# Optimization experiments

Hardware: AMD Instinct MI355X
Metric: run time of the kernel (lower is better)

## Reference

```python
import jax, jax.numpy as jnp
import numpy as np

B, N, DIM = 2, 2048, 1024
NUM_HEADS = 16
EFF = NUM_HEADS // 2          # 8 effective heads
HD = DIM // NUM_HEADS         # 64
LAMBDA_INIT = 0.8
EPS = 1e-5


def setup_inputs() -> dict:
    key = jax.random.key(0)
    ks = jax.random.split(key, 16)
    s = 0.02
    return {
        "x":  jax.random.normal(ks[0], (B, N, DIM), dtype=jnp.float32),
        "Wq": jax.random.normal(ks[1], (DIM, DIM), dtype=jnp.float32) * s,
        "bq": jnp.zeros((DIM,), dtype=jnp.float32),
        "Wk": jax.random.normal(ks[2], (DIM, DIM), dtype=jnp.float32) * s,
        "bk": jnp.zeros((DIM,), dtype=jnp.float32),
        "Wv": jax.random.normal(ks[3], (DIM, DIM), dtype=jnp.float32) * s,
        "bv": jnp.zeros((DIM,), dtype=jnp.float32),
        "Wo": jax.random.normal(ks[4], (DIM, DIM), dtype=jnp.float32) * s,
        "bo": jnp.zeros((DIM,), dtype=jnp.float32),
        "norm_w": jnp.ones((2 * HD,), dtype=jnp.float32),
        "lq1": jax.random.normal(ks[5], (HD,), dtype=jnp.float32) * 0.1,
        "lk1": jax.random.normal(ks[6], (HD,), dtype=jnp.float32) * 0.1,
        "lq2": jax.random.normal(ks[7], (HD,), dtype=jnp.float32) * 0.1,
        "lk2": jax.random.normal(ks[8], (HD,), dtype=jnp.float32) * 0.1,
    }


def reference(x, Wq, bq, Wk, bk, Wv, bv, Wo, bo, norm_w, lq1, lk1, lq2, lk2):
    scale = HD ** -0.5
    # projections (torch Linear: y = x @ W.T + b)
    q = (x @ Wq.T + bq).reshape(B, N, NUM_HEADS, HD).transpose(0, 2, 1, 3) * scale  # [B,2E,N,hd]
    k = (x @ Wk.T + bk).reshape(B, N, NUM_HEADS, HD).transpose(0, 2, 1, 3)          # [B,2E,N,hd]
    v = (x @ Wv.T + bv).reshape(B, N, EFF, 2 * HD).transpose(0, 2, 1, 3)            # [B,E,N,2hd]

    scores = jnp.einsum('bhqd,bhkd->bhqk', q, k)              # [B,2E,N,N]
    probs = jax.nn.softmax(scores, axis=-1)
    probs = probs.reshape(B, EFF, 2, N, N)                    # pair consecutive heads

    lam = jnp.exp(jnp.sum(lq1 * lk1)) - jnp.exp(jnp.sum(lq2 * lk2)) + LAMBDA_INIT
    diff = probs[:, :, 0] - lam * probs[:, :, 1]              # [B,E,N,N]

    out = jnp.einsum('behk,bekd->behd'.replace('e','h').replace('hh','h') if False else 'bhqk,bhkd->bhqd', diff, v)  # [B,E,N,2hd]
    # headwise RMSNorm over last dim (2*hd)
    out = out * jax.lax.rsqrt(jnp.mean(out * out, axis=-1, keepdims=True) + EPS) * norm_w
    out = out * (1.0 - LAMBDA_INIT)

    out = out.transpose(0, 2, 1, 3).reshape(B, N, DIM)
    return out @ Wo.T + bo
```

## Files before the change

kernel.cpp:

```cpp
#include <hip/hip_runtime.h>
#include <hip/hip_bf16.h>

#define B_   2
#define N_   2048
#define DIM_ 1024
#define HD_  64
#define DV_  128

typedef __bf16 bf16;
typedef __bf16 bf16x8 __attribute__((ext_vector_type(8)));
typedef __bf16 bf16x4 __attribute__((ext_vector_type(4)));
typedef float  floatx4 __attribute__((ext_vector_type(4)));
typedef float  floatx16 __attribute__((ext_vector_type(16)));
typedef unsigned int uint;
typedef uint uint2v __attribute__((ext_vector_type(2)));
typedef uint uint4v __attribute__((ext_vector_type(4)));

#if __has_builtin(__builtin_amdgcn_exp2f)
#define EXP2(x) __builtin_amdgcn_exp2f(x)
#else
#define EXP2(x) exp2f(x)
#endif

#define QSCALE 0.1803368801111244f

__device__ __forceinline__ void async16(const void* g, void* l) {
  __builtin_amdgcn_global_load_lds(
      (__attribute__((address_space(1))) void*)g,
      (__attribute__((address_space(3))) void*)l, 16, 0, 0);
}

__device__ __forceinline__ uint packbf(float a, float b) {
  unsigned short ul = __builtin_bit_cast(unsigned short, (bf16)a);
  unsigned short uh = __builtin_bit_cast(unsigned short, (bf16)b);
  return (uint)ul | ((uint)uh << 16);
}

__global__ void convert_kernel(const float* __restrict__ x,
                               const float* __restrict__ wq,
                               const float* __restrict__ wk,
                               const float* __restrict__ wv,
                               const float* __restrict__ wo,
                               bf16* __restrict__ dst) {
  const int NX = B_ * N_ * DIM_;
  const int NW = DIM_ * DIM_;
  int i = (blockIdx.x * 256 + threadIdx.x) * 4;
  const float* src;
  int off;
  if (i < NX) { src = x; off = i; }
  else {
    int j = i - NX;
    int w = j >> 20;
    off = j & (NW - 1);
    src = (w == 0) ? wq : (w == 1) ? wk : (w == 2) ? wv : wo;
  }
  float4 v = *(const float4*)(src + off);
  bf16x4 o = { (bf16)v.x, (bf16)v.y, (bf16)v.z, (bf16)v.w };
  *(bf16x4*)(dst + i) = o;
}

__global__ void lam_kernel(const float* __restrict__ lq1, const float* __restrict__ lk1,
                           const float* __restrict__ lq2, const float* __restrict__ lk2,
                           float* __restrict__ lam_out) {
  int l = threadIdx.x;
  float a = lq1[l] * lk1[l];
  float b = lq2[l] * lk2[l];
  for (int m = 1; m < 64; m <<= 1) {
    a += __shfl_xor(a, m, 64);
    b += __shfl_xor(b, m, 64);
  }
  if (l == 0) *lam_out = __expf(a) - __expf(b) + 0.8f;
}

__global__ __launch_bounds__(256) void proj_kernel(
    const bf16* __restrict__ xb, const bf16* __restrict__ wall,
    const float* __restrict__ bq, const float* __restrict__ bk,
    const float* __restrict__ bv,
    bf16* __restrict__ qo, bf16* __restrict__ ko, bf16* __restrict__ vt) {
  __shared__ __align__(16) bf16 SM[2 * 128 * 64];
  bf16* At = SM;
  bf16* Bt = SM + 128 * 64;
  const int tid = threadIdx.x, lane = tid & 63, w = tid >> 6;
  const int tm = blockIdx.x, tn = blockIdx.y, z = blockIdx.z;
  const int quad = lane >> 4, l15 = lane & 15;
  const int wm = (w >> 1) * 64, wn = (w & 1) * 64;
  const bf16* Ab = xb + (long)tm * 128 * DIM_;
  const bf16* Bb = wall + (long)z * (DIM_ * DIM_) + (long)tn * 128 * DIM_;
  floatx4 zero = {0.f, 0.f, 0.f, 0.f};
  floatx4 acc[4][4];
#pragma unroll
  for (int i = 0; i < 4; ++i)
#pragma unroll
    for (int j = 0; j < 4; ++j) acc[i][j] = zero;

  for (int kb = 0; kb < DIM_ / 64; ++kb) {
    for (int idx = tid; idx < 1024; idx += 256) {
      int row = idx >> 3, ch = idx & 7, g = ch ^ (row & 7);
      async16(Ab + row * DIM_ + kb * 64 + g * 8, (char*)At + (idx - lane) * 16);
      async16(Bb + row * DIM_ + kb * 64 + g * 8, (char*)Bt + (idx - lane) * 16);
    }
    __syncthreads();
#pragma unroll
    for (int ks = 0; ks < 2; ++ks) {
      bf16x8 af[4], bfm[4];
#pragma unroll
      for (int mt = 0; mt < 4; ++mt) {
        int r = wm + mt * 16 + l15;
        af[mt] = *(const bf16x8*)&At[r * 64 + ((ks * 4 + quad) ^ (r & 7)) * 8];
      }
#pragma unroll
      for (int nt = 0; nt < 4; ++nt) {
        int r = wn + nt * 16 + l15;
        bfm[nt] = *(const bf16x8*)&Bt[r * 64 + ((ks * 4 + quad) ^ (r & 7)) * 8];
      }
#pragma unroll
      for (int mt = 0; mt < 4; ++mt)
#pragma unroll
        for (int nt = 0; nt < 4; ++nt)
          acc[mt][nt] = __builtin_amdgcn_mfma_f32_16x16x32_bf16(
              af[mt], bfm[nt], acc[mt][nt], 0, 0, 0);
    }
    __syncthreads();
  }

  if (z != 2) {
#pragma unroll
    for (int mt = 0; mt < 4; ++mt)
#pragma unroll
      for (int nt = 0; nt < 4; ++nt)
#pragma unroll
        for (int r = 0; r < 4; ++r) {
          int grow = tm * 128 + wm + mt * 16 + quad * 4 + r;
          int gcol = tn * 128 + wn + nt * 16 + l15;
          float v = acc[mt][nt][r];
          if (z == 0) {
            qo[(long)grow * DIM_ + gcol] = (bf16)((v + bq[gcol]) * QSCALE);
          } else {
            ko[(long)grow * DIM_ + gcol] = (bf16)(v + bk[gcol]);
          }
        }
  } else {
    bf16* Vl = SM;
#pragma unroll
    for (int nt = 0; nt < 4; ++nt) {
      int d = wn + nt * 16 + l15;
      float bvv = bv[tn * 128 + d];
      int m = (d & 7) * 2;
#pragma unroll
      for (int mt = 0; mt < 4; ++mt) {
        bf16x4 v4 = { (bf16)(acc[mt][nt][0] + bvv), (bf16)(acc[mt][nt][1] + bvv),
                      (bf16)(acc[mt][nt][2] + bvv), (bf16)(acc[mt][nt][3] + bvv) };
        int c = (wm >> 2) + mt * 4 + quad;
        *(bf16x4*)&Vl[d * 128 + (c ^ m) * 4] = v4;
      }
    }
    __syncthreads();
    const int bb = tm >> 4, e = tn;
    const long rowbase = ((long)(bb * 8 + e) * 128) * (long)N_ + (tm & 15) * 128;
#pragma unroll
    for (int p = 0; p < 8; ++p) {
      int d = p * 16 + (tid >> 4), j = tid & 15;
      int cs = (2 * j) ^ ((d & 7) * 2);
      bf16x8 val = *(const bf16x8*)&Vl[d * 128 + cs * 4];
      *(bf16x8*)&vt[rowbase + (long)d * N_ + j * 8] = val;
    }
  }
}

__global__ __launch_bounds__(1024, 4) void attn_kernel(
    const bf16* __restrict__ qb, const bf16* __restrict__ kbuf,
    const bf16* __restrict__ vt, const float* __restrict__ lamp,
    const float* __restrict__ norm_w, bf16* __restrict__ ao) {
  __shared__ __align__(16) char smem[131072];
  __shared__ float Ls[512];

  const int tid = threadIdx.x, lane = tid & 63, w = tid >> 6;
  const int qt = blockIdx.x, e = blockIdx.y, b = blockIdx.z;
  const int hl = w & 1, qh = (w >> 1) & 3, cp = w >> 3;
  const int h = lane >> 5, l31 = lane & 31;
  const int qbase = qt * 128;

  bf16x8 qf[4];
  {
    const bf16* qrp = qb + (long)(b * N_ + qbase + qh * 32 + l31) * DIM_
                      + e * 128 + hl * 64 + h * 8;
#pragma unroll
    for (int c = 0; c < 4; ++c) qf[c] = *(const bf16x8*)(qrp + c * 16);
  }

  const bf16* kbase = kbuf + (long)b * N_ * DIM_ + e * 128;
  const bf16* vbase = vt + (long)(b * 8 + e) * DV_ * N_;

  floatx16 acc[4];
#pragma unroll
  for (int dt = 0; dt < 4; ++dt) acc[dt] = floatx16{};
  float lp = 0.f;

#define STAGE(ktv, bufv)                                                            \
  {                                                                                 \
    int kt_ = (ktv);                                                                \
    char* kdst = smem + (bufv) * 16384;                                             \
    char* vdst = smem + 32768 + (bufv) * 16384;                                     \
    {                                                                               \
      int idx = tid;                                                                \
      int khl = idx >> 9, row = (idx >> 3) & 63, ch = idx & 7;                      \
      int g = ch ^ (row & 7) ^ ((row >> 3) & 3);                                    \
      async16(kbase + ((long)(kt_ * 64 + row)) * DIM_ + khl * 64 + g * 8,           \
              kdst + (idx - lane) * 16);                                            \
    }                                                                               \
    {                                                                               \
      int idx = tid;                                                                \
      int row = idx >> 3, ch = idx & 7;                                             \
      int g = ch ^ (row & 7) ^ ((row >> 3) & 3);                                    \
      async16(vbase + (long)row * N_ + kt_ * 64 + g * 8,                            \
              vdst + (idx - lane) * 16);                                            \
    }                                                                               \
  }

  STAGE(0, 0);

  for (int kt = 0; kt < N_ / 64; ++kt) {
    const int buf = kt & 1;
    __syncthreads();
    if (kt + 1 < N_ / 64) STAGE(kt + 1, buf ^ 1);

    const bf16* Kh = (const bf16*)(smem + buf * 16384) + hl * 4096;
    const bf16* Vb = (const bf16*)(smem + 32768 + buf * 16384);

    bf16x8 kfrag[4], vfrag[4][2];
#pragma unroll
    for (int c = 0; c < 4; ++c) {
      int row = cp * 32 + l31;
      int sw = (c * 2 + h) ^ (row & 7) ^ ((row >> 3) & 3);
      kfrag[c] = *(const bf16x8*)&Kh[row * 64 + sw * 8];
    }
#pragma unroll
    for (int dt = 0; dt < 4; ++dt)
#pragma unroll
      for (int u = 0; u < 2; ++u) {
        int kc = cp * 2 + u;
        int row = dt * 32 + l31;
        int sw = (kc * 2 + h) ^ (row & 7) ^ ((row >> 3) & 3);
        vfrag[dt][u] = *(const bf16x8*)&Vb[row * 64 + sw * 8];
      }

    floatx16 sv{};
#pragma unroll
    for (int c = 0; c < 4; ++c)
      sv = __builtin_amdgcn_mfma_f32_32x32x16_bf16(kfrag[c], qf[c], sv, 0, 0, 0);
    float t[16];
    float s = 0.f;
#pragma unroll
    for (int i = 0; i < 16; ++i) { t[i] = EXP2(sv[i]); s += t[i]; }
    lp += s;
    uint d0 = packbf(t[0], t[1]),   d1 = packbf(t[2], t[3]);
    uint d2 = packbf(t[4], t[5]),   d3 = packbf(t[6], t[7]);
    uint d4 = packbf(t[8], t[9]),   d5 = packbf(t[10], t[11]);
    uint d6 = packbf(t[12], t[13]), d7 = packbf(t[14], t[15]);
    uint4v f0, f1;
#if __has_builtin(__builtin_amdgcn_permlane32_swap)
    uint2v r02 = __builtin_amdgcn_permlane32_swap(d0, d2, false, false);
    uint2v r13 = __builtin_amdgcn_permlane32_swap(d1, d3, false, false);
    f0 = uint4v{r02.x, r13.x, r02.y, r13.y};
    uint2v r46 = __builtin_amdgcn_permlane32_swap(d4, d6, false, false);
    uint2v r57 = __builtin_amdgcn_permlane32_swap(d5, d7, false, false);
    f1 = uint4v{r46.x, r57.x, r46.y, r57.y};
#else
    uint e0 = __shfl_xor((int)d0, 32, 64), e1 = __shfl_xor((int)d1, 32, 64);
    uint e2 = __shfl_xor((int)d2, 32, 64), e3 = __shfl_xor((int)d3, 32, 64);
    uint e4 = __shfl_xor((int)d4, 32, 64), e5 = __shfl_xor((int)d5, 32, 64);
    uint e6 = __shfl_xor((int)d6, 32, 64), e7 = __shfl_xor((int)d7, 32, 64);
    f0 = h ? uint4v{e2, e3, d2, d3} : uint4v{d0, d1, e0, e1};
    f1 = h ? uint4v{e6, e7, d6, d7} : uint4v{d4, d5, e4, e5};
#endif
    bf16x8 af0 = __builtin_bit_cast(bf16x8, f0);
    bf16x8 af1 = __builtin_bit_cast(bf16x8, f1);
#pragma unroll
    for (int dt = 0; dt < 4; ++dt) {
      acc[dt] = __builtin_amdgcn_mfma_f32_32x32x16_bf16(af0, vfrag[dt][0], acc[dt], 0, 0, 0);
      acc[dt] = __builtin_amdgcn_mfma_f32_32x32x16_bf16(af1, vfrag[dt][1], acc[dt], 0, 0, 0);
    }
  }

  lp += __shfl_xor(lp, 32, 64);
  if (h == 0) Ls[cp * 256 + hl * 128 + qh * 32 + l31] = lp;
  __syncthreads();
  float lptot = Ls[hl * 128 + qh * 32 + l31] + Ls[256 + hl * 128 + qh * 32 + l31];

  float* S = (float*)smem;
  float* T = (float*)(smem + 65536);

  if (hl == 1 && cp == 0) {
#pragma unroll
    for (int r = 0; r < 16; ++r) {
      int qloc = (r & 3) + 8 * (r >> 2) + 4 * h;
      float inv = 1.0f / __shfl(lptot, qloc, 64);
      float* row = &S[(qh * 32 + qloc) * 128 + l31];
#pragma unroll
      for (int dt = 0; dt < 4; ++dt) row[dt * 32] = acc[dt][r] * inv;
    }
  }
  if (hl == 0 && cp == 1) {
#pragma unroll
    for (int r = 0; r < 16; ++r) {
      int qloc = (r & 3) + 8 * (r >> 2) + 4 * h;
      float inv = 1.0f / __shfl(lptot, qloc, 64);
      float* row = &T[(qh * 32 + qloc) * 128 + l31];
#pragma unroll
      for (int dt = 0; dt < 4; ++dt) row[dt * 32] = acc[dt][r] * inv;
    }
  }
  __syncthreads();
  if (hl == 1 && cp == 1) {
#pragma unroll
    for (int r = 0; r < 16; ++r) {
      int qloc = (r & 3) + 8 * (r >> 2) + 4 * h;
      float inv = 1.0f / __shfl(lptot, qloc, 64);
      float* row = &S[(qh * 32 + qloc) * 128 + l31];
#pragma unroll
      for (int dt = 0; dt < 4; ++dt) row[dt * 32] += acc[dt][r] * inv;
    }
  }
  if (hl == 0 && cp == 0) {
#pragma unroll
    for (int r = 0; r < 16; ++r) {
      int qloc = (r & 3) + 8 * (r >> 2) + 4 * h;
      float inv = 1.0f / __shfl(lptot, qloc, 64);
      const float* row = &T[(qh * 32 + qloc) * 128 + l31];
#pragma unroll
      for (int dt = 0; dt < 4; ++dt) acc[dt][r] = acc[dt][r] * inv + row[dt * 32];
    }
  }
  __syncthreads();
  if (hl == 0 && cp == 0) {
    float lam = *lamp;
    float nw4[4];
#pragma unroll
    for (int dt = 0; dt < 4; ++dt) nw4[dt] = norm_w[dt * 32 + l31] * 0.2f;
#pragma unroll
    for (int r = 0; r < 16; ++r) {
      int qloc = (r & 3) + 8 * (r >> 2) + 4 * h;
      const float* row = &S[(qh * 32 + qloc) * 128 + l31];
      float v[4], ss = 0.f;
#pragma unroll
      for (int dt = 0; dt < 4; ++dt) {
        v[dt] = acc[dt][r] - lam * row[dt * 32];
        ss += v[dt] * v[dt];
      }
#pragma unroll
      for (int msk = 1; msk < 32; msk <<= 1) ss += __shfl_xor(ss, msk, 64);
      float rms = rsqrtf(ss * (1.0f / 128.0f) + 1e-5f);
      int n = qbase + qh * 32 + qloc;
      bf16* dst = ao + (long)(b * N_ + n) * DIM_ + e * DV_ + l31;
#pragma unroll
      for (int dt = 0; dt < 4; ++dt) dst[dt * 32] = (bf16)(v[dt] * rms * nw4[dt]);
    }
  }
}

__global__ __launch_bounds__(512) void out_gemm(
    const bf16* __restrict__ ab, const bf16* __restrict__ wo,
    const float* __restrict__ bo, float* __restrict__ out) {
  __shared__ __align__(16) bf16 At[128 * 64];
  __shared__ __align__(16) bf16 Bt[128 * 64];
  const int tid = threadIdx.x, lane = tid & 63, w = tid >> 6;
  const int tm = blockIdx.x, tn = blockIdx.y;
  const int quad = lane >> 4, l15 = lane & 15;
  const int wm = (w & 3) * 32, wn = (w >> 2) * 64;
  const bf16* Ab = ab + (long)tm * 128 * DIM_;
  const bf16* Bb = wo + (long)tn * 128 * DIM_;
  floatx4 zero = {0.f, 0.f, 0.f, 0.f};
  floatx4 acc[2][4];
#pragma unroll
  for (int i = 0; i < 2; ++i)
#pragma unroll
    for (int j = 0; j < 4; ++j) acc[i][j] = zero;

  for (int kb = 0; kb < DIM_ / 64; ++kb) {
    for (int idx = tid; idx < 1024; idx += 512) {
      int row = idx >> 3, ch = idx & 7, g = ch ^ (row & 7);
      async16(Ab + row * DIM_ + kb * 64 + g * 8, (char*)At + (idx - lane) * 16);
      async16(Bb + row * DIM_ + kb * 64 + g * 8, (char*)Bt + (idx - lane) * 16);
    }
    __syncthreads();
#pragma unroll
    for (int ks = 0; ks < 2; ++ks) {
      bf16x8 af[2], bfm[4];
#pragma unroll
      for (int mt = 0; mt < 2; ++mt) {
        int r = wm + mt * 16 + l15;
        af[mt] = *(const bf16x8*)&At[r * 64 + ((ks * 4 + quad) ^ (r & 7)) * 8];
      }
#pragma unroll
      for (int nt = 0; nt < 4; ++nt) {
        int r = wn + nt * 16 + l15;
        bfm[nt] = *(const bf16x8*)&Bt[r * 64 + ((ks * 4 + quad) ^ (r & 7)) * 8];
      }
#pragma unroll
      for (int mt = 0; mt < 2; ++mt)
#pragma unroll
        for (int nt = 0; nt < 4; ++nt)
          acc[mt][nt] = __builtin_amdgcn_mfma_f32_16x16x32_bf16(
              af[mt], bfm[nt], acc[mt][nt], 0, 0, 0);
    }
    __syncthreads();
  }
#pragma unroll
  for (int mt = 0; mt < 2; ++mt)
#pragma unroll
    for (int nt = 0; nt < 4; ++nt)
#pragma unroll
      for (int r = 0; r < 4; ++r) {
        int grow = tm * 128 + wm + mt * 16 + quad * 4 + r;
        int gcol = tn * 128 + wn + nt * 16 + l15;
        out[(long)grow * DIM_ + gcol] = acc[mt][nt][r] + bo[gcol];
      }
}

extern "C" void kernel_launch(void* const* d_in, const int* in_sizes, int n_in,
                              void* d_out, int out_size, void* d_ws, size_t ws_size,
                              hipStream_t stream) {
  const float* x    = (const float*)d_in[0];
  const float* Wq   = (const float*)d_in[1];
  const float* bq   = (const float*)d_in[2];
  const float* Wk   = (const float*)d_in[3];
  const float* bk   = (const float*)d_in[4];
  const float* Wv   = (const float*)d_in[5];
  const float* bv   = (const float*)d_in[6];
  const float* Wo   = (const float*)d_in[7];
  const float* bo   = (const float*)d_in[8];
  const float* nw   = (const float*)d_in[9];
  const float* lq1  = (const float*)d_in[10];
  const float* lk1  = (const float*)d_in[11];
  const float* lq2  = (const float*)d_in[12];
  const float* lk2  = (const float*)d_in[13];

  char* ws = (char*)d_ws;
  float* lam = (float*)ws;
  bf16* xb   = (bf16*)(ws + 256);
  bf16* wqb  = xb + 4194304;
  bf16* qb   = wqb + 4 * 1048576;
  bf16* kbuf = qb + 4194304;
  bf16* vtb  = kbuf + 4194304;
  bf16* ab   = vtb + 4194304;

  convert_kernel<<<8192, 256, 0, stream>>>(x, Wq, Wk, Wv, Wo, xb);
  lam_kernel<<<1, 64, 0, stream>>>(lq1, lk1, lq2, lk2, lam);
  proj_kernel<<<dim3(32, 8, 3), 256, 0, stream>>>(xb, wqb, bq, bk, bv, qb, kbuf, vtb);
  attn_kernel<<<dim3(16, 8, 2), 1024, 0, stream>>>(qb, kbuf, vtb, lam, nw, ab);
  out_gemm<<<dim3(32, 8), 512, 0, stream>>>(ab, wqb + 3 * 1048576, bo, (float*)d_out);
}
```

Measured before the change: 217.7 us.

## Halve attention block to 512 threads, each wave handling two query subtiles

The attention kernel drops from 16 to 8 waves per block, and each wave now processes two 32-row query subtiles against the same K/V fragments loaded from LDS. This amortizes the LDS fragment reads across twice the MFMA work and halves the number of waves contending for barriers. In exchange, each wave holds twice the accumulator and Q registers, which may limit occupancy or cause spills. The grid stays at 256 blocks, so there are fewer total waves to hide latency.

```diff
diff --git a/kernel.cpp b/kernel.cpp
--- a/kernel.cpp
+++ b/kernel.cpp
@@ -167,7 +167,7 @@
   }
 }
 
-__global__ __launch_bounds__(1024, 4) void attn_kernel(
+__global__ __launch_bounds__(512, 2) void attn_kernel(
     const bf16* __restrict__ qb, const bf16* __restrict__ kbuf,
     const bf16* __restrict__ vt, const float* __restrict__ lamp,
     const float* __restrict__ norm_w, bf16* __restrict__ ao) {
@@ -176,40 +176,43 @@
 
   const int tid = threadIdx.x, lane = tid & 63, w = tid >> 6;
   const int qt = blockIdx.x, e = blockIdx.y, b = blockIdx.z;
-  const int hl = w & 1, qh = (w >> 1) & 3, cp = w >> 3;
+  const int hl = w & 1, qh = (w >> 1) & 1, cp = w >> 2;
   const int h = lane >> 5, l31 = lane & 31;
   const int qbase = qt * 128;
 
-  bf16x8 qf[4];
-  {
-    const bf16* qrp = qb + (long)(b * N_ + qbase + qh * 32 + l31) * DIM_
+  bf16x8 qf[2][4];
+#pragma unroll
+  for (int qs = 0; qs < 2; ++qs) {
+    const bf16* qrp = qb + (long)(b * N_ + qbase + qh * 64 + qs * 32 + l31) * DIM_
                       + e * 128 + hl * 64 + h * 8;
 #pragma unroll
-    for (int c = 0; c < 4; ++c) qf[c] = *(const bf16x8*)(qrp + c * 16);
+    for (int c = 0; c < 4; ++c) qf[qs][c] = *(const bf16x8*)(qrp + c * 16);
   }
 
   const bf16* kbase = kbuf + (long)b * N_ * DIM_ + e * 128;
   const bf16* vbase = vt + (long)(b * 8 + e) * DV_ * N_;
 
-  floatx16 acc[4];
-#pragma unroll
-  for (int dt = 0; dt < 4; ++dt) acc[dt] = floatx16{};
-  float lp = 0.f;
+  floatx16 acc[2][4];
+#pragma unroll
+  for (int qs = 0; qs < 2; ++qs)
+#pragma unroll
+    for (int dt = 0; dt < 4; ++dt) acc[qs][dt] = floatx16{};
+  float lp[2] = {0.f, 0.f};
 
 #define STAGE(ktv, bufv)                                                            \
   {                                                                                 \
     int kt_ = (ktv);                                                                \
     char* kdst = smem + (bufv) * 16384;                                             \
     char* vdst = smem + 32768 + (bufv) * 16384;                                     \
-    {                                                                               \
-      int idx = tid;                                                                \
+    _Pragma("unroll") for (int t = 0; t < 2; ++t) {                                 \
+      int idx = tid + t * 512;                                                      \
       int khl = idx >> 9, row = (idx >> 3) & 63, ch = idx & 7;                      \
       int g = ch ^ (row & 7) ^ ((row >> 3) & 3);                                    \
       async16(kbase + ((long)(kt_ * 64 + row)) * DIM_ + khl * 64 + g * 8,           \
               kdst + (idx - lane) * 16);                                            \
     }                                                                               \
-    {                                                                               \
-      int idx = tid;                                                                \
+    _Pragma("unroll") for (int t = 0; t < 2; ++t) {                                 \
+      int idx = tid + t * 512;                                                      \
       int row = idx >> 3, ch = idx & 7;                                             \
       int g = ch ^ (row & 7) ^ ((row >> 3) & 3);                                    \
       async16(vbase + (long)row * N_ + kt_ * 64 + g * 8,                            \
@@ -244,92 +247,111 @@
         vfrag[dt][u] = *(const bf16x8*)&Vb[row * 64 + sw * 8];
       }
 
-    floatx16 sv{};
-#pragma unroll
-    for (int c = 0; c < 4; ++c)
-      sv = __builtin_amdgcn_mfma_f32_32x32x16_bf16(kfrag[c], qf[c], sv, 0, 0, 0);
-    float t[16];
-    float s = 0.f;
-#pragma unroll
-    for (int i = 0; i < 16; ++i) { t[i] = EXP2(sv[i]); s += t[i]; }
-    lp += s;
-    uint d0 = packbf(t[0], t[1]),   d1 = packbf(t[2], t[3]);
-    uint d2 = packbf(t[4], t[5]),   d3 = packbf(t[6], t[7]);
-    uint d4 = packbf(t[8], t[9]),   d5 = packbf(t[10], t[11]);
-    uint d6 = packbf(t[12], t[13]), d7 = packbf(t[14], t[15]);
-    uint4v f0, f1;
+#pragma unroll
+    for (int qs = 0; qs < 2; ++qs) {
+      floatx16 sv{};
+#pragma unroll
+      for (int c = 0; c < 4; ++c)
+        sv = __builtin_amdgcn_mfma_f32_32x32x16_bf16(kfrag[c], qf[qs][c], sv, 0, 0, 0);
+      float t[16];
+      float s = 0.f;
+#pragma unroll
+      for (int i = 0; i < 16; ++i) { t[i] = EXP2(sv[i]); s += t[i]; }
+      lp[qs] += s;
+      uint d0 = packbf(t[0], t[1]),   d1 = packbf(t[2], t[3]);
+      uint d2 = packbf(t[4], t[5]),   d3 = packbf(t[6], t[7]);
+      uint d4 = packbf(t[8], t[9]),   d5 = packbf(t[10], t[11]);
+      uint d6 = packbf(t[12], t[13]), d7 = packbf(t[14], t[15]);
+      uint4v f0, f1;
 #if __has_builtin(__builtin_amdgcn_permlane32_swap)
-    uint2v r02 = __builtin_amdgcn_permlane32_swap(d0, d2, false, false);
-    uint2v r13 = __builtin_amdgcn_permlane32_swap(d1, d3, false, false);
-    f0 = uint4v{r02.x, r13.x, r02.y, r13.y};
-    uint2v r46 = __builtin_amdgcn_permlane32_swap(d4, d6, false, false);
-    uint2v r57 = __builtin_amdgcn_permlane32_swap(d5, d7, false, false);
-    f1 = uint4v{r46.x, r57.x, r46.y, r57.y};
+      uint2v r02 = __builtin_amdgcn_permlane32_swap(d0, d2, false, false);
+      uint2v r13 = __builtin_amdgcn_permlane32_swap(d1, d3, false, false);
+      f0 = uint4v{r02.x, r13.x, r02.y, r13.y};
+      uint2v r46 = __builtin_amdgcn_permlane32_swap(d4, d6, false, false);
+      uint2v r57 = __builtin_amdgcn_permlane32_swap(d5, d7, false, false);
+      f1 = uint4v{r46.x, r57.x, r46.y, r57.y};
 #else
-    uint e0 = __shfl_xor((int)d0, 32, 64), e1 = __shfl_xor((int)d1, 32, 64);
-    uint e2 = __shfl_xor((int)d2, 32, 64), e3 = __shfl_xor((int)d3, 32, 64);
-    uint e4 = __shfl_xor((int)d4, 32, 64), e5 = __shfl_xor((int)d5, 32, 64);
-    uint e6 = __shfl_xor((int)d6, 32, 64), e7 = __shfl_xor((int)d7, 32, 64);
-    f0 = h ? uint4v{e2, e3, d2, d3} : uint4v{d0, d1, e0, e1};
-    f1 = h ? uint4v{e6, e7, d6, d7} : uint4v{d4, d5, e4, e5};
+      uint e0 = __shfl_xor((int)d0, 32, 64), e1 = __shfl_xor((int)d1, 32, 64);
+      uint e2 = __shfl_xor((int)d2, 32, 64), e3 = __shfl_xor((int)d3, 32, 64);
+      uint e4 = __shfl_xor((int)d4, 32, 64), e5 = __shfl_xor((int)d5, 32, 64);
+      uint e6 = __shfl_xor((int)d6, 32, 64), e7 = __shfl_xor((int)d7, 32, 64);
+      f0 = h ? uint4v{e2, e3, d2, d3} : uint4v{d0, d1, e0, e1};
+      f1 = h ? uint4v{e6, e7, d6, d7} : uint4v{d4, d5, e4, e5};
 #endif
-    bf16x8 af0 = __builtin_bit_cast(bf16x8, f0);
-    bf16x8 af1 = __builtin_bit_cast(bf16x8, f1);
-#pragma unroll
-    for (int dt = 0; dt < 4; ++dt) {
-      acc[dt] = __builtin_amdgcn_mfma_f32_32x32x16_bf16(af0, vfrag[dt][0], acc[dt], 0, 0, 0);
-      acc[dt] = __builtin_amdgcn_mfma_f32_32x32x16_bf16(af1, vfrag[dt][1], acc[dt], 0, 0, 0);
-    }
-  }
-
-  lp += __shfl_xor(lp, 32, 64);
-  if (h == 0) Ls[cp * 256 + hl * 128 + qh * 32 + l31] = lp;
+      bf16x8 af0 = __builtin_bit_cast(bf16x8, f0);
+      bf16x8 af1 = __builtin_bit_cast(bf16x8, f1);
+#pragma unroll
+      for (int dt = 0; dt < 4; ++dt) {
+        acc[qs][dt] = __builtin_amdgcn_mfma_f32_32x32x16_bf16(af0, vfrag[dt][0], acc[qs][dt], 0, 0, 0);
+        acc[qs][dt] = __builtin_amdgcn_mfma_f32_32x32x16_bf16(af1, vfrag[dt][1], acc[qs][dt], 0, 0, 0);
+      }
+    }
+  }
+
+  lp[0] += __shfl_xor(lp[0], 32, 64);
+  lp[1] += __shfl_xor(lp[1], 32, 64);
+  if (h == 0) {
+    Ls[cp * 256 + hl * 128 + qh * 64 + 0 * 32 + l31] = lp[0];
+    Ls[cp * 256 + hl * 128 + qh * 64 + 1 * 32 + l31] = lp[1];
+  }
   __syncthreads();
-  float lptot = Ls[hl * 128 + qh * 32 + l31] + Ls[256 + hl * 128 + qh * 32 + l31];
+  float lptot[2];
+#pragma unroll
+  for (int qs = 0; qs < 2; ++qs)
+    lptot[qs] = Ls[hl * 128 + qh * 64 + qs * 32 + l31]
+              + Ls[256 + hl * 128 + qh * 64 + qs * 32 + l31];
 
   float* S = (float*)smem;
   float* T = (float*)(smem + 65536);
 
   if (hl == 1 && cp == 0) {
 #pragma unroll
-    for (int r = 0; r < 16; ++r) {
-      int qloc = (r & 3) + 8 * (r >> 2) + 4 * h;
-      float inv = 1.0f / __shfl(lptot, qloc, 64);
-      float* row = &S[(qh * 32 + qloc) * 128 + l31];
-#pragma unroll
-      for (int dt = 0; dt < 4; ++dt) row[dt * 32] = acc[dt][r] * inv;
-    }
+    for (int qs = 0; qs < 2; ++qs)
+#pragma unroll
+      for (int r = 0; r < 16; ++r) {
+        int qloc = (r & 3) + 8 * (r >> 2) + 4 * h;
+        float inv = 1.0f / __shfl(lptot[qs], qloc, 64);
+        float* row = &S[(qh * 64 + qs * 32 + qloc) * 128 + l31];
+#pragma unroll
+        for (int dt = 0; dt < 4; ++dt) row[dt * 32] = acc[qs][dt][r] * inv;
+      }
   }
   if (hl == 0 && cp == 1) {
 #pragma unroll
-    for (int r = 0; r < 16; ++r) {
-      int qloc = (r & 3) + 8 * (r >> 2) + 4 * h;
-      float inv = 1.0f / __shfl(lptot, qloc, 64);
-      float* row = &T[(qh * 32 + qloc) * 128 + l31];
-#pragma unroll
-      for (int dt = 0; dt < 4; ++dt) row[dt * 32] = acc[dt][r] * inv;
-    }
+    for (int qs = 0; qs < 2; ++qs)
+#pragma unroll
+      for (int r = 0; r < 16; ++r) {
+        int qloc = (r & 3) + 8 * (r >> 2) + 4 * h;
+        float inv = 1.0f / __shfl(lptot[qs], qloc, 64);
+        float* row = &T[(qh * 64 + qs * 32 + qloc) * 128 + l31];
+#pragma unroll
+        for (int dt = 0; dt < 4; ++dt) row[dt * 32] = acc[qs][dt][r] * inv;
+      }
   }
   __syncthreads();
   if (hl == 1 && cp == 1) {
 #pragma unroll
-    for (int r = 0; r < 16; ++r) {
-      int qloc = (r & 3) + 8 * (r >> 2) + 4 * h;
-      float inv = 1.0f / __shfl(lptot, qloc, 64);
-      float* row = &S[(qh * 32 + qloc) * 128 + l31];
-#pragma unroll
-      for (int dt = 0; dt < 4; ++dt) row[dt * 32] += acc[dt][r] * inv;
-    }
+    for (int qs = 0; qs < 2; ++qs)
+#pragma unroll
+      for (int r = 0; r < 16; ++r) {
+        int qloc = (r & 3) + 8 * (r >> 2) + 4 * h;
+        float inv = 1.0f / __shfl(lptot[qs], qloc, 64);
+        float* row = &S[(qh * 64 + qs * 32 + qloc) * 128 + l31];
+#pragma unroll
+        for (int dt = 0; dt < 4; ++dt) row[dt * 32] += acc[qs][dt][r] * inv;
+      }
   }
   if (hl == 0 && cp == 0) {
 #pragma unroll
-    for (int r = 0; r < 16; ++r) {
-      int qloc = (r & 3) + 8 * (r >> 2) + 4 * h;
-      float inv = 1.0f / __shfl(lptot, qloc, 64);
-      const float* row = &T[(qh * 32 + qloc) * 128 + l31];
-#pragma unroll
-      for (int dt = 0; dt < 4; ++dt) acc[dt][r] = acc[dt][r] * inv + row[dt * 32];
-    }
+    for (int qs = 0; qs < 2; ++qs)
+#pragma unroll
+      for (int r = 0; r < 16; ++r) {
+        int qloc = (r & 3) + 8 * (r >> 2) + 4 * h;
+        float inv = 1.0f / __shfl(lptot[qs], qloc, 64);
+        const float* row = &T[(qh * 64 + qs * 32 + qloc) * 128 + l31];
+#pragma unroll
+        for (int dt = 0; dt < 4; ++dt) acc[qs][dt][r] = acc[qs][dt][r] * inv + row[dt * 32];
+      }
   }
   __syncthreads();
   if (hl == 0 && cp == 0) {
@@ -338,23 +360,25 @@
 #pragma unroll
     for (int dt = 0; dt < 4; ++dt) nw4[dt] = norm_w[dt * 32 + l31] * 0.2f;
 #pragma unroll
-    for (int r = 0; r < 16; ++r) {
-      int qloc = (r & 3) + 8 * (r >> 2) + 4 * h;
-      const float* row = &S[(qh * 32 + qloc) * 128 + l31];
-      float v[4], ss = 0.f;
-#pragma unroll
-      for (int dt = 0; dt < 4; ++dt) {
-        v[dt] = acc[dt][r] - lam * row[dt * 32];
-        ss += v[dt] * v[dt];
-      }
-#pragma unroll
-      for (int msk = 1; msk < 32; msk <<= 1) ss += __shfl_xor(ss, msk, 64);
-      float rms = rsqrtf(ss * (1.0f / 128.0f) + 1e-5f);
-      int n = qbase + qh * 32 + qloc;
-      bf16* dst = ao + (long)(b * N_ + n) * DIM_ + e * DV_ + l31;
-#pragma unroll
-      for (int dt = 0; dt < 4; ++dt) dst[dt * 32] = (bf16)(v[dt] * rms * nw4[dt]);
-    }
+    for (int qs = 0; qs < 2; ++qs)
+#pragma unroll
+      for (int r = 0; r < 16; ++r) {
+        int qloc = (r & 3) + 8 * (r >> 2) + 4 * h;
+        const float* row = &S[(qh * 64 + qs * 32 + qloc) * 128 + l31];
+        float v[4], ss = 0.f;
+#pragma unroll
+        for (int dt = 0; dt < 4; ++dt) {
+          v[dt] = acc[qs][dt][r] - lam * row[dt * 32];
+          ss += v[dt] * v[dt];
+        }
+#pragma unroll
+        for (int msk = 1; msk < 32; msk <<= 1) ss += __shfl_xor(ss, msk, 64);
+        float rms = rsqrtf(ss * (1.0f / 128.0f) + 1e-5f);
+        int n = qbase + qh * 64 + qs * 32 + qloc;
+        bf16* dst = ao + (long)(b * N_ + n) * DIM_ + e * DV_ + l31;
+#pragma unroll
+        for (int dt = 0; dt < 4; ++dt) dst[dt * 32] = (bf16)(v[dt] * rms * nw4[dt]);
+      }
   }
 }
 
@@ -447,6 +471,6 @@
   convert_kernel<<<8192, 256, 0, stream>>>(x, Wq, Wk, Wv, Wo, xb);
   lam_kernel<<<1, 64, 0, stream>>>(lq1, lk1, lq2, lk2, lam);
   proj_kernel<<<dim3(32, 8, 3), 256, 0, stream>>>(xb, wqb, bq, bk, bv, qb, kbuf, vtb);
-  attn_kernel<<<dim3(16, 8, 2), 1024, 0, stream>>>(qb, kbuf, vtb, lam, nw, ab);
+  attn_kernel<<<dim3(16, 8, 2), 512, 0, stream>>>(qb, kbuf, vtb, lam, nw, ab);
   out_gemm<<<dim3(32, 8), 512, 0, stream>>>(ab, wqb + 3 * 1048576, bo, (float*)d_out);
 }
```

New measurement: 222.8 us. +2.4%, slower.
